# Kernel optimization log

Measured on AMD Instinct MI355X. Metric: run time of the kernel, lower is better.

Reference implementation:

```python
import jax, jax.numpy as jnp
import numpy as np
from jax.scipy.special import logsumexp

TAU = 0.05
ITERATIONS = 10


def setup_inputs() -> dict:
    key = jax.random.key(0)
    logits = jax.random.normal(key, (256, 512, 512), dtype=jnp.float32)
    return {"logits": logits}


def reference(logits) -> jnp.ndarray:
    # log-space Sinkhorn-Knopp: project logits/tau to a doubly stochastic matrix
    Z = logits / TAU  # [B, n, n]
    u0 = jnp.zeros(Z.shape[:-1], dtype=Z.dtype)  # [B, n] row potentials
    v0 = jnp.zeros_like(u0)                      # [B, n] col potentials
    # log_marginal is zeros(n) in the original, i.e. uniform target marginals of 1

    def body(_, uv):
        u, v = uv
        u = -logsumexp(Z + v[..., None, :], axis=-1)  # row normalization
        v = -logsumexp(Z + u[..., :, None], axis=-2)  # col normalization
        return (u, v)

    u, v = jax.lax.fori_loop(0, ITERATIONS, body, (u0, v0))
    return jnp.exp(Z + u[..., :, None] + v[..., None, :])
```

## Files before the change

kernel.cpp:

```cpp
#include <hip/hip_runtime.h>

#define BN 512
#define NW 16
#define RPW 32
#define LR  7

static constexpr float kScale = 28.853900817779268f;

__device__ __forceinline__ float fexp2(float x){ return __builtin_amdgcn_exp2f(x); }
__device__ __forceinline__ float flog2(float x){ return __builtin_amdgcn_logf(x); }
__device__ __forceinline__ float frcp (float x){ return __builtin_amdgcn_rcpf(x); }

__device__ __forceinline__ float dpp_sum64(float s){
    int t;
    t = __builtin_amdgcn_update_dpp(0, __float_as_int(s), 0x111, 0xf, 0xf, true); s += __int_as_float(t);
    t = __builtin_amdgcn_update_dpp(0, __float_as_int(s), 0x112, 0xf, 0xf, true); s += __int_as_float(t);
    t = __builtin_amdgcn_update_dpp(0, __float_as_int(s), 0x114, 0xf, 0xf, true); s += __int_as_float(t);
    t = __builtin_amdgcn_update_dpp(0, __float_as_int(s), 0x118, 0xf, 0xf, true); s += __int_as_float(t);
    t = __builtin_amdgcn_update_dpp(0, __float_as_int(s), 0x142, 0xa, 0xf, true); s += __int_as_float(t);
    t = __builtin_amdgcn_update_dpp(0, __float_as_int(s), 0x143, 0xc, 0xf, true); s += __int_as_float(t);
    return __int_as_float(__builtin_amdgcn_readlane(__float_as_int(s), 63));
}
__device__ __forceinline__ float dpp_max64(float m){
    const int NI = __float_as_int(-__builtin_inff());
    int t;
    t = __builtin_amdgcn_update_dpp(NI, __float_as_int(m), 0x111, 0xf, 0xf, false); m = fmaxf(m, __int_as_float(t));
    t = __builtin_amdgcn_update_dpp(NI, __float_as_int(m), 0x112, 0xf, 0xf, false); m = fmaxf(m, __int_as_float(t));
    t = __builtin_amdgcn_update_dpp(NI, __float_as_int(m), 0x114, 0xf, 0xf, false); m = fmaxf(m, __int_as_float(t));
    t = __builtin_amdgcn_update_dpp(NI, __float_as_int(m), 0x118, 0xf, 0xf, false); m = fmaxf(m, __int_as_float(t));
    t = __builtin_amdgcn_update_dpp(NI, __float_as_int(m), 0x142, 0xa, 0xf, false); m = fmaxf(m, __int_as_float(t));
    t = __builtin_amdgcn_update_dpp(NI, __float_as_int(m), 0x143, 0xc, 0xf, false); m = fmaxf(m, __int_as_float(t));
    return __int_as_float(__builtin_amdgcn_readlane(__float_as_int(m), 63));
}

__device__ __forceinline__ unsigned rtne_pack(float a, float b){
    unsigned ua = __float_as_uint(a), ub = __float_as_uint(b);
    unsigned lo = (ua + 0x7fffu + ((ua >> 16) & 1u)) >> 16;
    unsigned hi = (ub + 0x7fffu + ((ub >> 16) & 1u)) & 0xffff0000u;
    return lo | hi;
}
__device__ __forceinline__ void unpack2(unsigned w, float& lo, float& hi){
    lo = __uint_as_float(w << 16);
    hi = __uint_as_float(w & 0xffff0000u);
}

__device__ __forceinline__ int credIdx(int p){
    return ((p >> 8) * 288) + (((p & 255) >> 3) * 9) + (p & 7);
}

__global__ __launch_bounds__(1024, 1) void sinkhorn_fused(
    const float* __restrict__ logits, float* __restrict__ out,
    unsigned short* __restrict__ ws, int use_ws)
{
    __shared__ float Bf[BN];
    __shared__ float SL[BN];
    __shared__ float cred[NW][576];
    __shared__ unsigned short Mlds[NW * LR * BN];

    const int b = blockIdx.x;
    const size_t base = (size_t)b * BN * BN;
    const float* __restrict__ Zb = logits + base;
    float* __restrict__ Ob = out + base;
    unsigned short* __restrict__ Mb = use_ws ? (ws + base) : (unsigned short*)Ob;

    const int tid  = threadIdx.x;
    const int lane = tid & 63;
    const int wave = tid >> 6;
    const int wb   = wave * RPW;

    {
        float ca[8] = {0.f,0.f,0.f,0.f,0.f,0.f,0.f,0.f};

        #pragma unroll 2
        for (int r = 0; r < RPW; ++r) {
            const int i = wb + r;
            const float4 x0 = *reinterpret_cast<const float4*>(Zb + (size_t)i * BN + 4 * lane);
            const float4 x1 = *reinterpret_cast<const float4*>(Zb + (size_t)i * BN + 256 + 4 * lane);

            float t[8];
            t[0] = x0.x * kScale; t[1] = x0.y * kScale; t[2] = x0.z * kScale; t[3] = x0.w * kScale;
            t[4] = x1.x * kScale; t[5] = x1.y * kScale; t[6] = x1.z * kScale; t[7] = x1.w * kScale;

            float m = t[0];
            #pragma unroll
            for (int k = 1; k < 8; ++k) m = fmaxf(m, t[k]);
            m = dpp_max64(m);

            float p[8], s = 0.f;
            #pragma unroll
            for (int k = 0; k < 8; ++k) { p[k] = fexp2(t[k] - m); s += p[k]; }
            s = dpp_sum64(s);

            const float f = fexp2(64.0f - flog2(s));
            float Mv[8];
            #pragma unroll
            for (int k = 0; k < 8; ++k) { Mv[k] = p[k] * f; ca[k] += Mv[k]; }

            int4 packed;
            packed.x = (int)rtne_pack(Mv[0], Mv[1]);
            packed.y = (int)rtne_pack(Mv[2], Mv[3]);
            packed.z = (int)rtne_pack(Mv[4], Mv[5]);
            packed.w = (int)rtne_pack(Mv[6], Mv[7]);
            if (r < LR)
                *reinterpret_cast<int4*>(&Mlds[(wave * LR + r) * BN + lane * 8]) = packed;
            else
                *reinterpret_cast<int4*>(Mb + (size_t)i * BN + lane * 8) = packed;
        }

        const int cbase = (lane < 32) ? lane * 9 : 288 + (lane - 32) * 9;
        #pragma unroll
        for (int k = 0; k < 8; ++k) cred[wave][cbase + k] = ca[k];
        __syncthreads();
    }

    const unsigned short* Mw = Mb + (size_t)wb * BN + lane * 8;
#define LD(r)  (*reinterpret_cast<const int4*>(Mw + (size_t)(r) * BN))
#define LDL(r) (*reinterpret_cast<const int4*>(&Mlds[(wave * LR + (r)) * BN + lane * 8]))

    int4 W0 = LD(7), W1 = LD(8), W2 = LD(9), W3 = LD(10);

    if (tid < BN) {
        const int ci = credIdx(tid);
        float s = 0.f;
        #pragma unroll
        for (int wv = 0; wv < NW; ++wv) s += cred[wv][ci];
        Bf[tid] = frcp(s);
    }
    __syncthreads();

#define STEP1(ridx, W)                                                             \
    {                                                                              \
        float e[8];                                                                \
        unpack2((unsigned)(W).x, e[0], e[1]); unpack2((unsigned)(W).y, e[2], e[3]); \
        unpack2((unsigned)(W).z, e[4], e[5]); unpack2((unsigned)(W).w, e[6], e[7]); \
        float a0 = 0.f, a1 = 0.f, a2 = 0.f, a3 = 0.f;                              \
        a0 = fmaf(e[0], bl[0], a0); a1 = fmaf(e[1], bl[1], a1);                    \
        a2 = fmaf(e[2], bl[2], a2); a3 = fmaf(e[3], bl[3], a3);                    \
        a0 = fmaf(e[4], bl[4], a0); a1 = fmaf(e[5], bl[5], a1);                    \
        a2 = fmaf(e[6], bl[6], a2); a3 = fmaf(e[7], bl[7], a3);                    \
        const float s = dpp_sum64((a0 + a1) + (a2 + a3));                          \
        const float A = frcp(s);                                                   \
        if (lane == 0) SL[wb + (ridx)] = s;                                        \
        _Pragma("unroll")                                                          \
        for (int k = 0; k < 8; ++k) ca[k] = fmaf(e[k], A, ca[k]);                  \
    }

    for (int it = 1; it < 10; ++it) {
        float bl[8];
        #pragma unroll
        for (int k = 0; k < 8; ++k) bl[k] = Bf[8 * lane + k];
        float ca[8] = {0.f,0.f,0.f,0.f,0.f,0.f,0.f,0.f};

        {
            int4 V0 = LDL(0), V1 = LDL(1);
            STEP1(0, V0); V0 = LDL(2);
            STEP1(1, V1); V1 = LDL(3);
            STEP1(2, V0); V0 = LDL(4);
            STEP1(3, V1); V1 = LDL(5);
            STEP1(4, V0); V0 = LDL(6);
            STEP1(5, V1);
            STEP1(6, V0);
        }

        #pragma unroll 1
        for (int g = 0; g < 20; g += 4) {
            STEP1(7 + g,  W0); W0 = LD(11 + g);
            STEP1(8 + g,  W1); W1 = LD(12 + g);
            STEP1(9 + g,  W2); W2 = LD(13 + g);
            STEP1(10 + g, W3); W3 = LD(14 + g);
        }
        STEP1(27, W0); W0 = LD(31);
        STEP1(28, W1); W1 = LD(8);
        STEP1(29, W2); W2 = LD(9);
        STEP1(30, W3); W3 = LD(10);
        STEP1(31, W0); W0 = LD(7);

        const int cbase = (lane < 32) ? lane * 9 : 288 + (lane - 32) * 9;
        #pragma unroll
        for (int k = 0; k < 8; ++k) cred[wave][cbase + k] = ca[k];
        __syncthreads();
        if (tid < BN) {
            const int ci = credIdx(tid);
            float s = 0.f;
            #pragma unroll
            for (int wv = 0; wv < NW; ++wv) s += cred[wv][ci];
            Bf[tid] = frcp(s);
        }
        __syncthreads();
    }

    {
        float bf[8];
        #pragma unroll
        for (int k = 0; k < 8; ++k) bf[k] = Bf[8 * lane + k];

        auto emit_row = [&](int j) {
            const int lr = j & 31;
            const int4 w = (lr < LR)
                ? *reinterpret_cast<const int4*>(&Mlds[((j >> 5) * LR + lr) * BN + lane * 8])
                : *reinterpret_cast<const int4*>(Mb + (size_t)j * BN + lane * 8);
            float e[8];
            unpack2((unsigned)w.x, e[0], e[1]); unpack2((unsigned)w.y, e[2], e[3]);
            unpack2((unsigned)w.z, e[4], e[5]); unpack2((unsigned)w.w, e[6], e[7]);
            const float A = frcp(SL[j]);
            float4 o0, o1;
            o0.x = e[0] * A * bf[0]; o0.y = e[1] * A * bf[1];
            o0.z = e[2] * A * bf[2]; o0.w = e[3] * A * bf[3];
            o1.x = e[4] * A * bf[4]; o1.y = e[5] * A * bf[5];
            o1.z = e[6] * A * bf[6]; o1.w = e[7] * A * bf[7];
            *reinterpret_cast<float4*>(Ob + (size_t)j * BN + 4 * lane) = o0;
            *reinterpret_cast<float4*>(Ob + (size_t)j * BN + 256 + 4 * lane) = o1;
        };

        if (use_ws) {
            #pragma unroll 2
            for (int r = 0; r < RPW; ++r) emit_row(wb + r);
        } else {
            for (int L = 256; L >= 1; L >>= 1) {
                for (int j = L + wave; j < 2 * L; j += NW) emit_row(j);
                __syncthreads();
            }
            if (wave == 0) emit_row(0);
        }
    }
#undef LD
#undef LDL
#undef STEP1
}

extern "C" void kernel_launch(void* const* d_in, const int* in_sizes, int n_in,
                              void* d_out, int out_size, void* d_ws, size_t ws_size,
                              hipStream_t stream) {
    const float* logits = (const float*)d_in[0];
    float* out = (float*)d_out;
    const int B = in_sizes[0] / (BN * BN);
    const size_t need = (size_t)B * BN * BN * sizeof(unsigned short);
    const int use_ws = (ws_size >= need) ? 1 : 0;
    hipLaunchKernelGGL(sinkhorn_fused, dim3(B), dim3(1024), 0, stream,
                       logits, out, (unsigned short*)d_ws, use_ws);
}
```

Measured before the change: 263.6 us.

## Replace column-sum staging buffer with LDS atomics and cache more rows in LDS

The per-wave column-partial buffer (16x576 floats) and its 16-way serial reduction are replaced by a 512-float accumulator that each lane updates with LDS atomicAdd, using a rotated index to spread bank conflicts. The LDS space this frees lets each wave keep 9 instead of 7 of its 32 bf16 rows resident in LDS, so fewer rows are re-read from global memory on each iteration. The register prefetch schedule is reworked to match, and the final-iteration prefetch is skipped. LDS atomics add contention and make the floating-point summation order nondeterministic.

```diff
diff --git a/kernel.cpp b/kernel.cpp
--- a/kernel.cpp
+++ b/kernel.cpp
@@ -3,7 +3,7 @@
 #define BN 512
 #define NW 16
 #define RPW 32
-#define LR  7
+#define LR  9
 
 static constexpr float kScale = 28.853900817779268f;
 
@@ -44,17 +44,13 @@
     hi = __uint_as_float(w & 0xffff0000u);
 }
 
-__device__ __forceinline__ int credIdx(int p){
-    return ((p >> 8) * 288) + (((p & 255) >> 3) * 9) + (p & 7);
-}
-
 __global__ __launch_bounds__(1024, 1) void sinkhorn_fused(
     const float* __restrict__ logits, float* __restrict__ out,
     unsigned short* __restrict__ ws, int use_ws)
 {
     __shared__ float Bf[BN];
     __shared__ float SL[BN];
-    __shared__ float cred[NW][576];
+    __shared__ float Cn[BN];
     __shared__ unsigned short Mlds[NW * LR * BN];
 
     const int b = blockIdx.x;
@@ -67,6 +63,18 @@
     const int lane = tid & 63;
     const int wave = tid >> 6;
     const int wb   = wave * RPW;
+
+    if (tid < BN) Cn[tid] = 0.0f;
+    __syncthreads();
+
+#define COL_ATOMIC(ca)                                                             \
+    {                                                                              \
+        _Pragma("unroll")                                                          \
+        for (int k = 0; k < 8; ++k) {                                              \
+            const int idx = ((lane >> 2) + k) & 7;                                 \
+            atomicAdd(&Cn[8 * lane + idx], (ca)[idx]);                             \
+        }                                                                          \
+    }
 
     {
         float ca[8] = {0.f,0.f,0.f,0.f,0.f,0.f,0.f,0.f};
@@ -107,9 +115,7 @@
                 *reinterpret_cast<int4*>(Mb + (size_t)i * BN + lane * 8) = packed;
         }
 
-        const int cbase = (lane < 32) ? lane * 9 : 288 + (lane - 32) * 9;
-        #pragma unroll
-        for (int k = 0; k < 8; ++k) cred[wave][cbase + k] = ca[k];
+        COL_ATOMIC(ca);
         __syncthreads();
     }
 
@@ -117,15 +123,9 @@
 #define LD(r)  (*reinterpret_cast<const int4*>(Mw + (size_t)(r) * BN))
 #define LDL(r) (*reinterpret_cast<const int4*>(&Mlds[(wave * LR + (r)) * BN + lane * 8]))
 
-    int4 W0 = LD(7), W1 = LD(8), W2 = LD(9), W3 = LD(10);
-
-    if (tid < BN) {
-        const int ci = credIdx(tid);
-        float s = 0.f;
-        #pragma unroll
-        for (int wv = 0; wv < NW; ++wv) s += cred[wv][ci];
-        Bf[tid] = frcp(s);
-    }
+    int4 W0 = LD(9), W1 = LD(10), W2 = LD(11), W3 = LD(12);
+
+    if (tid < BN) { Bf[tid] = frcp(Cn[tid]); Cn[tid] = 0.0f; }
     __syncthreads();
 
 #define STEP1(ridx, W)                                                             \
@@ -158,34 +158,31 @@
             STEP1(2, V0); V0 = LDL(4);
             STEP1(3, V1); V1 = LDL(5);
             STEP1(4, V0); V0 = LDL(6);
-            STEP1(5, V1);
-            STEP1(6, V0);
+            STEP1(5, V1); V1 = LDL(7);
+            STEP1(6, V0); V0 = LDL(8);
+            STEP1(7, V1);
+            STEP1(8, V0);
         }
 
         #pragma unroll 1
-        for (int g = 0; g < 20; g += 4) {
-            STEP1(7 + g,  W0); W0 = LD(11 + g);
-            STEP1(8 + g,  W1); W1 = LD(12 + g);
-            STEP1(9 + g,  W2); W2 = LD(13 + g);
-            STEP1(10 + g, W3); W3 = LD(14 + g);
-        }
-        STEP1(27, W0); W0 = LD(31);
-        STEP1(28, W1); W1 = LD(8);
-        STEP1(29, W2); W2 = LD(9);
-        STEP1(30, W3); W3 = LD(10);
-        STEP1(31, W0); W0 = LD(7);
-
-        const int cbase = (lane < 32) ? lane * 9 : 288 + (lane - 32) * 9;
-        #pragma unroll
-        for (int k = 0; k < 8; ++k) cred[wave][cbase + k] = ca[k];
+        for (int g = 0; g < 16; g += 4) {
+            STEP1(9 + g,  W0); W0 = LD(13 + g);
+            STEP1(10 + g, W1); W1 = LD(14 + g);
+            STEP1(11 + g, W2); W2 = LD(15 + g);
+            STEP1(12 + g, W3); W3 = LD(16 + g);
+        }
+        STEP1(25, W0); W0 = LD(29);
+        STEP1(26, W1); W1 = LD(30);
+        STEP1(27, W2); W2 = LD(31);
+        STEP1(28, W3);
+        STEP1(29, W0);
+        STEP1(30, W1);
+        STEP1(31, W2);
+        if (it != 9) { W0 = LD(9); W1 = LD(10); W2 = LD(11); W3 = LD(12); }
+
+        COL_ATOMIC(ca);
         __syncthreads();
-        if (tid < BN) {
-            const int ci = credIdx(tid);
-            float s = 0.f;
-            #pragma unroll
-            for (int wv = 0; wv < NW; ++wv) s += cred[wv][ci];
-            Bf[tid] = frcp(s);
-        }
+        if (tid < BN) { Bf[tid] = frcp(Cn[tid]); Cn[tid] = 0.0f; }
         __syncthreads();
     }
 
@@ -226,6 +223,7 @@
 #undef LD
 #undef LDL
 #undef STEP1
+#undef COL_ATOMIC
 }
 
 extern "C" void kernel_launch(void* const* d_in, const int* in_sizes, int n_in,
```

After: 354.3 us. 1.34x slower.
